# Performance work log

Measured on AMD Instinct MI355X. Metric: run time of the kernel, lower is better.

## Reference

```python
import jax, jax.numpy as jnp
import numpy as np

MEAN = 0.1307
SIGMA = 0.3081
BINARY_ITER = 10
SIG_SCALE = 5.0


def spu(x):
    # SPU(x) = x^2 - 0.5 for x >= 0, sigmoid(-x) - 1 for x < 0 (continuous at 0)
    return jnp.where(x >= 0, x * x - 0.5, jax.nn.sigmoid(-x) - 1.0)


def joining_line(x1, y1, x2, y2):
    slope = (y2 - y1) / (x2 - x1)
    return slope, y2 - slope * x2


def parabola_tangent(x):
    return 2.0 * x, -x * x - 0.5


def parabola_tangent_through(x1, y1):
    D = 4.0 * x1 * x1 - 4.0 * y1 - 2.0
    x2 = (2.0 * x1 + jnp.sqrt(jnp.clip(D, 0.0))) / 2.0
    return parabola_tangent(x2)


def sigmoid_tangent(x):
    s = jax.nn.sigmoid(x)
    slope = -s * (1.0 - s)
    return slope, -s - slope * x


def binary_search_point(lx, ux, uy):
    L = lx
    R = jnp.zeros_like(lx)
    for _ in range(BINARY_ITER):  # fixed 10-iteration search, unrolled
        m = 0.5 * (L + R)
        sm, im = sigmoid_tangent(m)
        mask = sm * ux + im - uy > 0
        L = jnp.where(mask, m, L)
        R = jnp.where(mask, R, m)
    return L


def line_to_constraint(slope, intercept):
    # [n, n+1]: diagonal slope matrix with intercept as last column (matches torch diagflat/cat)
    return jnp.concatenate([jnp.diagflat(slope), intercept[:, None]], axis=1)


def analyze_affine(W, b, ub, lb):
    constr = jnp.concatenate([W, b[:, None]], axis=1)
    bu = jnp.where(W > 0, ub[None, :], lb[None, :])
    bl = jnp.where(W > 0, lb[None, :], ub[None, :])
    return constr, jnp.einsum('ij,ij->i', bu, W) + b, jnp.einsum('ij,ij->i', bl, W) + b


def analyze_spu(ux, lx):
    uy = spu(ux)
    ly = spu(lx)
    new_ub = jnp.maximum(uy, ly)
    sj, ij = joining_line(lx, ly, ux, uy)
    right = lx > 0
    left = ux <= 0
    crossing = (~left) & (~right)
    # learned positions at their (fresh) init: sigmoid(0) -> midpoint
    mid = 0.5 * (ux + lx)
    sp, ip = parabola_tangent(mid)
    ssm, ism = sigmoid_tangent(mid)
    new_lb = jnp.where(crossing, jnp.full_like(uy, -0.5), jnp.minimum(uy, ly))
    # crossing-case lower constraint
    spu_, ipu = parabola_tangent(ux)
    limit = spu_ * lx + ipu
    clm = (jnp.abs(lx) > ux).astype(lx.dtype)
    clp = jax.nn.sigmoid((clm - 0.5) * 2.0 * SIG_SCALE) * (ly - limit) + limit
    ptm = clp < -0.5
    spt, ipt = parabola_tangent_through(lx, clp)
    sjn, ijn = joining_line(lx, clp, jnp.zeros_like(lx), jnp.full_like(lx, -0.5))
    s_cl = jnp.where(ptm, spt, sjn)
    i_cl = jnp.where(ptm, ipt, ijn)
    # crossing-case upper constraint
    ssl, isl = sigmoid_tangent(lx)
    stv = ssl * ux + isl - uy
    L = binary_search_point(lx, ux, uy)
    scp = jax.nn.sigmoid(-SIG_SCALE) * (L - lx) + lx
    ssc, isc = sigmoid_tangent(scp)
    up_mask = stv > 0
    s_cu = jnp.where(up_mask, ssc, sj)
    i_cu = jnp.where(up_mask, isc, ij)
    rf = right.astype(lx.dtype)
    lf = left.astype(lx.dtype)
    cf = crossing.astype(lx.dtype)
    us = rf * sj + lf * ssm + cf * s_cu
    ui = rf * ij + lf * ism + cf * i_cu
    ls = rf * sp + lf * sj + cf * s_cl
    li = rf * ip + lf * ij + cf * i_cl
    return line_to_constraint(us, ui), line_to_constraint(ls, li), new_ub, new_lb


def back_substitute(uc, lc, ub, lb):
    cu, cl = uc[-1], lc[-1]
    for pu, pl in zip(uc[-2::-1], lc[-2::-1]):
        # where(curr>0, prev_upper, prev_lower) contracted with curr == split pos/neg matmuls
        Wu, bu = cu[:, :-1], cu[:, -1]
        cu = jnp.maximum(Wu, 0.0) @ pu + jnp.minimum(Wu, 0.0) @ pl
        cu = cu.at[:, -1].add(bu)
        Wl, bl = cl[:, :-1], cl[:, -1]
        cl = jnp.maximum(Wl, 0.0) @ pl + jnp.minimum(Wl, 0.0) @ pu
        cl = cl.at[:, -1].add(bl)
    return jnp.minimum(ub, cu[:, 0]), jnp.maximum(lb, cl[:, 0])


def setup_inputs() -> dict:
    key = jax.random.key(0)
    ks = jax.random.split(key, 9)
    d_in, h, d_out = 784, 2048, 10
    inputs = jax.random.uniform(ks[0], (d_in,), dtype=jnp.float32)
    eps = jnp.float32(0.05)
    w1 = jax.random.normal(ks[1], (h, d_in), dtype=jnp.float32) / np.sqrt(d_in).astype(np.float32)
    b1 = jax.random.normal(ks[2], (h,), dtype=jnp.float32) * 0.1
    w2 = jax.random.normal(ks[3], (h, h), dtype=jnp.float32) / np.sqrt(h).astype(np.float32)
    b2 = jax.random.normal(ks[4], (h,), dtype=jnp.float32) * 0.1
    w3 = jax.random.normal(ks[5], (h, h), dtype=jnp.float32) / np.sqrt(h).astype(np.float32)
    b3 = jax.random.normal(ks[6], (h,), dtype=jnp.float32) * 0.1
    w4 = jax.random.normal(ks[7], (d_out, h), dtype=jnp.float32) / np.sqrt(h).astype(np.float32)
    b4 = jax.random.normal(ks[8], (d_out,), dtype=jnp.float32) * 0.1
    return {"inputs": inputs, "eps": eps, "w1": w1, "b1": b1, "w2": w2, "b2": b2,
            "w3": w3, "b3": b3, "w4": w4, "b4": b4}


def reference(inputs, eps, w1, b1, w2, b2, w3, b3, w4, b4):
    ub = [jnp.clip(inputs + eps, None, 1.0)]
    lb = [jnp.clip(inputs - eps, 0.0)]
    # normalization layer: applied in place to bounds and input constraint ([784,1])
    uc = [((ub[0] - MEAN) / SIGMA)[:, None]]
    lc = [((lb[0] - MEAN) / SIGMA)[:, None]]
    ub[0] = (ub[0] - MEAN) / SIGMA
    lb[0] = (lb[0] - MEAN) / SIGMA
    weights = [(w1, b1), (w2, b2), (w3, b3), (w4, b4)]
    for i, (W, b) in enumerate(weights):
        c, u, l = analyze_affine(W, b, ub[-1], lb[-1])
        uc.append(c)
        lc.append(c)
        ub.append(u)
        lb.append(l)
        u, l = back_substitute(uc, lc, ub[-1], lb[-1])
        ub[-1], lb[-1] = u, l
        if i < len(weights) - 1:
            cu_, cl_, u, l = analyze_spu(ub[-1], lb[-1])
            uc.append(cu_)
            lc.append(cl_)
            ub.append(u)
            lb.append(l)
            u, l = back_substitute(uc, lc, ub[-1], lb[-1])
            ub[-1], lb[-1] = u, l
    return lb[-1].min()
```

## Files before the change

kernel.cpp:

```cpp
#include <hip/hip_runtime.h>
#include <cstdint>
#include <cstddef>

#define MEAN_C 0.1307f
#define SIGMA_C 0.3081f
#define SIG_SCALE_C 5.0f

typedef __bf16 bf16_t;
typedef __bf16 bf16x8 __attribute__((ext_vector_type(8)));
typedef __bf16 bf16x4 __attribute__((ext_vector_type(4)));
typedef float f32x4 __attribute__((ext_vector_type(4)));

__device__ __forceinline__ f32x4 mfma16(bf16x8 a, bf16x8 b, f32x4 c) {
    return __builtin_amdgcn_mfma_f32_16x16x32_bf16(a, b, c, 0, 0, 0);
}

typedef const __attribute__((address_space(1))) void* gvp;
typedef __attribute__((address_space(3))) void* lvp;
__device__ __forceinline__ void g2l16(const void* g, void* l) {
    __builtin_amdgcn_global_load_lds((gvp)g, (lvp)l, 16, 0, 0);
}

__device__ __forceinline__ size_t swz(int r, int k, int ktiles) {
    return (((size_t)(r >> 4) * ktiles + (k >> 5)) << 9)
         + (((k >> 3) & 3) << 7) + ((r & 15) << 3) + (k & 7);
}

#define KTILES 64


__device__ __forceinline__ float sigmoidf_(float x) {
    if (x >= 0.f) { float e = __expf(-x); return 1.f / (1.f + e); }
    float e = __expf(x); return e / (1.f + e);
}

__device__ __forceinline__ float spu_f(float x) {
    return (x >= 0.f) ? (x * x - 0.5f) : (sigmoidf_(-x) - 1.f);
}

__device__ __forceinline__ float wave_sum(float a) {
    #pragma unroll
    for (int o = 32; o > 0; o >>= 1) a += __shfl_xor(a, o, 64);
    return a;
}

__device__ __forceinline__ void spu_body(int i, int n,
        float iUi, float iLi, float vU, float vL,
        float* __restrict__ us, float* __restrict__ ui,
        float* __restrict__ ls, float* __restrict__ li,
        float* __restrict__ pU, float* __restrict__ pL) {
    float ux = fminf(iUi, vU);
    float lx = fmaxf(iLi, vL);
    float uy = spu_f(ux), ly = spu_f(lx);
    float new_ub = fmaxf(uy, ly);
    float sj = (uy - ly) / (ux - lx);
    float ij = uy - sj * ux;
    bool right = lx > 0.f;
    bool left = ux <= 0.f;
    float mid = 0.5f * (ux + lx);
    float sp = 2.f * mid, ip = -mid * mid - 0.5f;
    float sm = sigmoidf_(mid);
    float ssm = -sm * (1.f - sm);
    float ism = -sm - ssm * mid;
    bool crossing = (!left) && (!right);
    float new_lb = crossing ? -0.5f : fminf(uy, ly);
    float spu_s = 2.f * ux, ipu = -ux * ux - 0.5f;
    float limit = spu_s * lx + ipu;
    float clm = (fabsf(lx) > ux) ? 1.f : 0.f;
    float clp = sigmoidf_((clm - 0.5f) * 2.f * SIG_SCALE_C) * (ly - limit) + limit;
    bool ptm = clp < -0.5f;
    float D = 4.f * lx * lx - 4.f * clp - 2.f;
    float x2 = (2.f * lx + sqrtf(fmaxf(D, 0.f))) * 0.5f;
    float spt = 2.f * x2, ipt = -x2 * x2 - 0.5f;
    float sjn = (clp + 0.5f) / lx;
    float ijn = -0.5f;
    float s_cl = ptm ? spt : sjn;
    float i_cl = ptm ? ipt : ijn;
    float sl = sigmoidf_(lx);
    float ssl = -sl * (1.f - sl);
    float isl = -sl - ssl * lx;
    float stv = ssl * ux + isl - uy;
    float Lb = lx, Rb = 0.f;
    #pragma unroll
    for (int t = 0; t < 10; ++t) {
        float mm = 0.5f * (Lb + Rb);
        float smm = sigmoidf_(mm);
        float sms = -smm * (1.f - smm);
        float smi = -smm - sms * mm;
        bool mask = (sms * ux + smi - uy) > 0.f;
        Lb = mask ? mm : Lb;
        Rb = mask ? Rb : mm;
    }
    float scp = sigmoidf_(-SIG_SCALE_C) * (Lb - lx) + lx;
    float sc = sigmoidf_(scp);
    float ssc = -sc * (1.f - sc);
    float isc = -sc - ssc * scp;
    bool up = stv > 0.f;
    float s_cu = up ? ssc : sj;
    float i_cu = up ? isc : ij;
    float usv, uiv, lsv, liv;
    if (right)      { usv = sj;   uiv = ij;   lsv = sp;   liv = ip;   }
    else if (left)  { usv = ssm;  uiv = ism;  lsv = sj;   liv = ij;   }
    else            { usv = s_cu; uiv = i_cu; lsv = s_cl; liv = i_cl; }
    us[i] = usv; ui[i] = uiv; ls[i] = lsv; li[i] = liv;
    float vu = (usv >= 0.f) ? vU : vL;
    float vl = (lsv >= 0.f) ? vL : vU;
    pU[i] = fminf(new_ub, usv * vu + uiv);
    pL[i] = fmaxf(new_lb, lsv * vl + liv);
}


__global__ __launch_bounds__(256) void k_interval_spu(
        const float* __restrict__ W, const float* __restrict__ b,
        const float* __restrict__ U, const float* __restrict__ L,
        int m, int n,
        float* __restrict__ us, float* __restrict__ ui,
        float* __restrict__ ls, float* __restrict__ li,
        float* __restrict__ pU, float* __restrict__ pL) {
    int r = (blockIdx.x << 2) + (threadIdx.x >> 6);
    if (r >= n) return;
    int lane = threadIdx.x & 63;
    const f32x4* Wr = (const f32x4*)(W + (size_t)r * m);
    const f32x4* U4 = (const f32x4*)U;
    const f32x4* L4 = (const f32x4*)L;
    int nf4 = m >> 2;
    float au = 0.f, al = 0.f;
    for (int j = lane; j < nf4; j += 64) {
        f32x4 wv = Wr[j], uu = U4[j], ll = L4[j];
        #pragma unroll
        for (int u = 0; u < 4; ++u) {
            float w = wv[u];
            float hi = (w > 0.f) ? uu[u] : ll[u];
            float lo2 = (w > 0.f) ? ll[u] : uu[u];
            au = fmaf(w, hi, au);
            al = fmaf(w, lo2, al);
        }
    }
    au = wave_sum(au); al = wave_sum(al);
    if (lane == 0) {
        float vU = au + b[r], vL = al + b[r];
        spu_body(r, n, vU, vL, vU, vL, us, ui, ls, li, pU, pL);
    }
}

__global__ void k_spu2(const float* __restrict__ iU, const float* __restrict__ iL,
                       const float* __restrict__ vraw, int n,
                       float* __restrict__ us, float* __restrict__ ui,
                       float* __restrict__ ls, float* __restrict__ li,
                       float* __restrict__ pU, float* __restrict__ pL) {
    int i = blockIdx.x * blockDim.x + threadIdx.x;
    if (i >= n) return;
    spu_body(i, n, iU[i], iL[i], vraw[i], vraw[n + i], us, ui, ls, li, pU, pL);
}


__global__ __launch_bounds__(256) void k_wT3(
        const float* __restrict__ W1, const float* __restrict__ W2,
        const float* __restrict__ W3,
        bf16_t* __restrict__ W1t, bf16_t* __restrict__ W2t, bf16_t* __restrict__ W3t,
        const float* __restrict__ x, const float* __restrict__ eps,
        float* __restrict__ ubn, float* __restrict__ lbn) {
    __shared__ bf16_t t[64 * 65];
    int z = blockIdx.z;
    const float* W; int N, ldw; bf16_t* Wt;
    if (z == 0)      { W = W2; N = 2048; ldw = 2048; Wt = W2t; }
    else if (z == 1) { W = W3; N = 2048; ldw = 2048; Wt = W3t; }
    else {
        W = W1; N = 784; ldw = 784; Wt = W1t;
        if (blockIdx.y >= 14) {
            if (blockIdx.y == 14 && blockIdx.x == 0) {
                for (int i = threadIdx.x; i < 896; i += 256) {
                    if (i >= 784) { ubn[i] = 0.f; lbn[i] = 0.f; }
                    else {
                        float e = eps[0];
                        float ub = fminf(x[i] + e, 1.f);
                        float lb = fmaxf(x[i] - e, 0.f);
                        ubn[i] = (ub - MEAN_C) / SIGMA_C;
                        lbn[i] = (lb - MEAN_C) / SIGMA_C;
                    }
                }
            }
            return;
        }
    }
    int k0 = blockIdx.x * 64, n0 = blockIdx.y * 64;
    int tid = threadIdx.x;
    int rg = tid >> 4;
    int cg = (tid & 15) * 4;
    bool fast = (n0 + 64 <= N);
    #pragma unroll
    for (int it = 0; it < 4; ++it) {
        int row = it * 16 + rg;
        const float* Wr = W + (size_t)(k0 + row) * ldw + n0 + cg;
        float v0, v1, v2, v3;
        if (fast) {
            f32x4 vv = *(const f32x4*)Wr;
            v0 = vv[0]; v1 = vv[1]; v2 = vv[2]; v3 = vv[3];
        } else {
            v0 = (n0 + cg + 0 < N) ? Wr[0] : 0.f;
            v1 = (n0 + cg + 1 < N) ? Wr[1] : 0.f;
            v2 = (n0 + cg + 2 < N) ? Wr[2] : 0.f;
            v3 = (n0 + cg + 3 < N) ? Wr[3] : 0.f;
        }
        t[(cg + 0) * 65 + row] = (bf16_t)v0;
        t[(cg + 1) * 65 + row] = (bf16_t)v1;
        t[(cg + 2) * 65 + row] = (bf16_t)v2;
        t[(cg + 3) * 65 + row] = (bf16_t)v3;
    }
    __syncthreads();
    #pragma unroll
    for (int p = 0; p < 2; ++p) {
        int c = tid + p * 256;
        int lr = c & 63, lq = c >> 6;
        bf16x8 v;
        #pragma unroll
        for (int u = 0; u < 8; ++u) v[u] = t[lr * 65 + lq * 8 + u];
        *(bf16x8*)(Wt + swz(n0 + lr, k0 + lq * 8, KTILES)) = v;
    }
}

__global__ __launch_bounds__(256) void k_prep16(
        const float* __restrict__ W, const float* __restrict__ b, int n,
        const float* __restrict__ cus, const float* __restrict__ cui,
        const float* __restrict__ cls, const float* __restrict__ cli,
        const float* __restrict__ bvec,
        const float* __restrict__ U, const float* __restrict__ L,
        bf16_t* __restrict__ Ab, float* __restrict__ av,
        float* __restrict__ iU, float* __restrict__ iL) {
    int rt = blockIdx.x;
    int tid = threadIdx.x, lane = tid & 63, wid = tid >> 6;
    int mrow = lane & 15, q = lane >> 4;
    int r = rt * 16 + mrow;
    bool act = r < 2 * n;
    bool isU = r < n;
    int i = act ? (isU ? r : r - n) : 0;
    float gate = act ? 1.f : 0.f;
    const float* Wr = W + (size_t)i * 2048;
    const float* ps = isU ? cus : cls;
    const float* ns = isU ? cls : cus;
    const float* yi = isU ? cui : cli;
    const float* zi = isU ? cli : cui;
    const float* hi = isU ? U : L;
    const float* lo = isU ? L : U;
    float a = 0.f, a2 = 0.f;
    bf16_t* Abase = Ab + ((size_t)rt * KTILES) * 512 + lane * 8;
    for (int kt = wid; kt < KTILES; kt += 4) {
        int k0 = kt * 32 + q * 8;
        bf16x8 ov;
        #pragma unroll
        for (int h = 0; h < 2; ++h) {
            int kb = k0 + 4 * h;
            f32x4 wv = *(const f32x4*)(Wr + kb);
            f32x4 p0 = *(const f32x4*)(ps + kb);
            f32x4 q0 = *(const f32x4*)(ns + kb);
            f32x4 y0 = *(const f32x4*)(yi + kb);
            f32x4 z0 = *(const f32x4*)(zi + kb);
            f32x4 c0 = *(const f32x4*)(bvec + kb);
            f32x4 h0 = *(const f32x4*)(hi + kb);
            f32x4 l0 = *(const f32x4*)(lo + kb);
            #pragma unroll
            for (int u = 0; u < 4; ++u) {
                float w = gate * wv[u];
                float pos = fmaxf(w, 0.f), neg = fminf(w, 0.f);
                float mx = pos * p0[u] + neg * q0[u];
                ov[4 * h + u] = (bf16_t)mx;
                a += pos * y0[u] + neg * z0[u] + mx * c0[u];
                a2 += pos * h0[u] + neg * l0[u];
            }
        }
        *(bf16x8*)(Abase + (size_t)kt * 512) = ov;
    }
    a += __shfl_xor(a, 16, 64);  a += __shfl_xor(a, 32, 64);
    a2 += __shfl_xor(a2, 16, 64); a2 += __shfl_xor(a2, 32, 64);
    __shared__ float sh[2][4][16];
    if (lane < 16) { sh[0][wid][lane] = a; sh[1][wid][lane] = a2; }
    __syncthreads();
    if (tid < 16) {
        int r2 = rt * 16 + tid;
        float ta = sh[0][0][tid] + sh[0][1][tid] + sh[0][2][tid] + sh[0][3][tid];
        float tb = sh[1][0][tid] + sh[1][1][tid] + sh[1][2][tid] + sh[1][3][tid];
        if (r2 < 2 * n) {
            bool isU2 = r2 < n;
            int i2 = isU2 ? r2 : r2 - n;
            av[r2] = ta + b[i2];
            if (isU2) iU[i2] = tb + b[i2];
            else      iL[i2] = tb + b[i2];
        } else {
            av[r2] = 0.f;
        }
    }
}

__global__ __launch_bounds__(256) void k_colmix16(
        const bf16_t* __restrict__ Cb, int ldc, int splits, size_t sstride, int n,
        int tpb,
        const float* __restrict__ cus, const float* __restrict__ cui,
        const float* __restrict__ cls, const float* __restrict__ cli,
        const float* __restrict__ bvec,
        bf16_t* __restrict__ Ab, float* __restrict__ av) {
    int rt = blockIdx.x;
    int kt0 = blockIdx.y * tpb;
    int tid = threadIdx.x, lane = tid & 63, wid = tid >> 6;
    int mrow = lane & 15, q = lane >> 4;
    int r = rt * 16 + mrow;
    bool isU = r < n;
    const bf16_t* Cr = Cb + (size_t)r * ldc;
    const float* ps = isU ? cus : cls;
    const float* ns = isU ? cls : cus;
    const float* yi = isU ? cui : cli;
    const float* zi = isU ? cli : cui;
    float a = 0.f;
    bf16_t* Abase = Ab + ((size_t)rt * KTILES) * 512 + lane * 8;
    for (int kt = kt0 + wid; kt < kt0 + tpb; kt += 4) {
        int k0 = kt * 32 + q * 8;
        float wsum[8] = {0.f, 0.f, 0.f, 0.f, 0.f, 0.f, 0.f, 0.f};
        for (int s = 0; s < splits; ++s) {
            bf16x8 v = *(const bf16x8*)(Cr + s * sstride + k0);
            #pragma unroll
            for (int u = 0; u < 8; ++u) wsum[u] += (float)v[u];
        }
        f32x4 p0 = *(const f32x4*)(ps + k0), p1 = *(const f32x4*)(ps + k0 + 4);
        f32x4 q0 = *(const f32x4*)(ns + k0), q1 = *(const f32x4*)(ns + k0 + 4);
        f32x4 y0 = *(const f32x4*)(yi + k0), y1 = *(const f32x4*)(yi + k0 + 4);
        f32x4 z0 = *(const f32x4*)(zi + k0), z1 = *(const f32x4*)(zi + k0 + 4);
        f32x4 c0 = *(const f32x4*)(bvec + k0), c1 = *(const f32x4*)(bvec + k0 + 4);
        bf16x8 ov;
        #pragma unroll
        for (int u = 0; u < 4; ++u) {
            float w = wsum[u];
            float pos = fmaxf(w, 0.f), neg = fminf(w, 0.f);
            float mx = pos * p0[u] + neg * q0[u];
            ov[u] = (bf16_t)mx;
            a += pos * y0[u] + neg * z0[u] + mx * c0[u];
        }
        #pragma unroll
        for (int u = 0; u < 4; ++u) {
            float w = wsum[4 + u];
            float pos = fmaxf(w, 0.f), neg = fminf(w, 0.f);
            float mx = pos * p1[u] + neg * q1[u];
            ov[4 + u] = (bf16_t)mx;
            a += pos * y1[u] + neg * z1[u] + mx * c1[u];
        }
        *(bf16x8*)(Abase + (size_t)kt * 512) = ov;
    }
    a += __shfl_xor(a, 16, 64);
    a += __shfl_xor(a, 32, 64);
    __shared__ float sh[4][16];
    if (lane < 16) sh[wid][lane] = a;
    __syncthreads();
    if (tid < 16) {
        float tot = sh[0][tid] + sh[1][tid] + sh[2][tid] + sh[3][tid];
        atomicAdd(&av[rt * 16 + tid], tot);
    }
}

__global__ __launch_bounds__(640) void k_reduce16f(
        const bf16_t* __restrict__ Cb, int ldc, int m, int n,
        int splits, size_t sstride,
        const float* __restrict__ av,
        const float* __restrict__ ubn, const float* __restrict__ lbn,
        const float* __restrict__ iL,
        float* __restrict__ out) {
    __shared__ float sbl[16];
    int tid = threadIdx.x, lane = tid & 63, wv = tid >> 6;
    int nch = m >> 3;
    int i = wv;
    int r = n + i;
    const bf16_t* Cr = Cb + (size_t)r * ldc;
    const float* p = lbn;
    const float* q = ubn;
    float a = 0.f;
    for (int c = lane; c < nch; c += 64) {
        float wsum[8] = {0.f, 0.f, 0.f, 0.f, 0.f, 0.f, 0.f, 0.f};
        for (int s = 0; s < splits; ++s) {
            bf16x8 v = *(const bf16x8*)(Cr + s * sstride + c * 8);
            #pragma unroll
            for (int u = 0; u < 8; ++u) wsum[u] += (float)v[u];
        }
        f32x4 p0 = *(const f32x4*)(p + c * 8), p1 = *(const f32x4*)(p + c * 8 + 4);
        f32x4 q0 = *(const f32x4*)(q + c * 8), q1 = *(const f32x4*)(q + c * 8 + 4);
        #pragma unroll
        for (int u = 0; u < 4; ++u) {
            a += fmaxf(wsum[u], 0.f) * p0[u] + fminf(wsum[u], 0.f) * q0[u];
            a += fmaxf(wsum[4 + u], 0.f) * p1[u] + fminf(wsum[4 + u], 0.f) * q1[u];
        }
    }
    a = wave_sum(a);
    if (lane == 0) sbl[i] = fmaxf(iL[i], a + av[r]);
    __syncthreads();
    if (tid < 64) {
        float v = 3.4e38f;
        for (int j = lane; j < n; j += 64) v = fminf(v, sbl[j]);
        #pragma unroll
        for (int o = 32; o > 0; o >>= 1) v = fminf(v, __shfl_down(v, o, 64));
        if (lane == 0) out[0] = v;
    }
}

#define GEMM_PIPE()                                                            \
    int tid = threadIdx.x, lane = tid & 63, w = tid >> 6;                      \
    int wm = w & 1, wn = w >> 1;                                               \
    f32x4 acc[4][4];                                                           \
    _Pragma("unroll")                                                          \
    for (int i = 0; i < 4; ++i)                                                \
        _Pragma("unroll")                                                      \
        for (int j = 0; j < 4; ++j) acc[i][j] = (f32x4){0.f, 0.f, 0.f, 0.f};   \
    auto stage = [&](int kk) {                                                 \
        int b = kk & 1;                                                        \
        size_t go = (size_t)kk * 1024;                                         \
        bf16_t* la = &As2[b * 8192 + w * 1024];                                \
        bf16_t* lb = &Bs2[b * 8192 + w * 1024];                                \
        g2l16(a0 + go, la);          g2l16(a0 + go + 512, la + 512);           \
        g2l16(a1 + go, la + 4096);   g2l16(a1 + go + 512, la + 4608);          \
        g2l16(b0 + go, lb);          g2l16(b0 + go + 512, lb + 512);           \
        g2l16(b1 + go, lb + 4096);   g2l16(b1 + go + 512, lb + 4608);          \
    };                                                                         \
    stage(0); stage(1);                                                        \
    asm volatile("s_waitcnt vmcnt(8)" ::: "memory");                           \
    __builtin_amdgcn_s_barrier();                                              \
    for (int kk = 0; kk < nk; ++kk) {                                          \
        const bf16_t* cA = &As2[(kk & 1) * 8192];                              \
        const bf16_t* cB = &Bs2[(kk & 1) * 8192];                              \
        bf16x8 af0[4], af1[4], bq0[4], bq1[4];                                 \
        _Pragma("unroll")                                                      \
        for (int i = 0; i < 4; ++i) {                                          \
            af0[i] = *(const bf16x8*)(cA + (wm * 4 + i) * 1024 + lane * 8);    \
            af1[i] = *(const bf16x8*)(cA + (wm * 4 + i) * 1024 + 512 + lane * 8); \
            bq0[i] = *(const bf16x8*)(cB + (wn * 4 + i) * 1024 + lane * 8);    \
            bq1[i] = *(const bf16x8*)(cB + (wn * 4 + i) * 1024 + 512 + lane * 8); \
        }                                                                      \
        asm volatile("s_waitcnt lgkmcnt(0)" ::: "memory");                     \
        __builtin_amdgcn_s_barrier();                                          \
        if (kk + 2 < nk) stage(kk + 2);                                        \
        _Pragma("unroll")                                                      \
        for (int i = 0; i < 4; ++i)                                            \
            _Pragma("unroll")                                                  \
            for (int j = 0; j < 4; ++j)                                        \
                acc[i][j] = mfma16(bq0[j], af0[i], acc[i][j]);                 \
        _Pragma("unroll")                                                      \
        for (int i = 0; i < 4; ++i)                                            \
            _Pragma("unroll")                                                  \
            for (int j = 0; j < 4; ++j)                                        \
                acc[i][j] = mfma16(bq1[j], af1[i], acc[i][j]);                 \
        if (kk + 2 < nk) asm volatile("s_waitcnt vmcnt(8)" ::: "memory");      \
        else             asm volatile("s_waitcnt vmcnt(0)" ::: "memory");      \
        __builtin_amdgcn_s_barrier();                                          \
    }

__global__ __launch_bounds__(256) void k_gemm16(
        const bf16_t* __restrict__ A, const bf16_t* __restrict__ Bt,
        bf16_t* __restrict__ C, int ldc, size_t sstride, int nk) {
    __shared__ __align__(16) bf16_t As2[16384];
    __shared__ __align__(16) bf16_t Bs2[16384];
    int tr0 = blockIdx.y * 8, tc0 = blockIdx.x * 8;
    int kt0 = blockIdx.z * nk * 2;
    int wtmp = threadIdx.x >> 6, ltmp = threadIdx.x & 63;
    const bf16_t* a0 = A + (((size_t)(tr0 + wtmp)     * KTILES + kt0) << 9) + ltmp * 8;
    const bf16_t* a1 = A + (((size_t)(tr0 + wtmp + 4) * KTILES + kt0) << 9) + ltmp * 8;
    const bf16_t* b0 = Bt + (((size_t)(tc0 + wtmp)     * KTILES + kt0) << 9) + ltmp * 8;
    const bf16_t* b1 = Bt + (((size_t)(tc0 + wtmp + 4) * KTILES + kt0) << 9) + ltmp * 8;
    GEMM_PIPE()
    bf16_t* Cz = C + (size_t)blockIdx.z * sstride;
    int orow = lane & 15, ocol = (lane >> 4) * 4;
    size_t row0 = (size_t)blockIdx.y * 128;
    size_t col0 = (size_t)blockIdx.x * 128;
    #pragma unroll
    for (int i = 0; i < 4; ++i) {
        size_t gr = row0 + wm * 64 + i * 16 + orow;
        #pragma unroll
        for (int j = 0; j < 4; ++j) {
            size_t gc = col0 + wn * 64 + j * 16 + ocol;
            bf16x4 v;
            #pragma unroll
            for (int rg = 0; rg < 4; ++rg) v[rg] = (bf16_t)acc[i][j][rg];
            *(bf16x4*)(Cz + gr * (size_t)ldc + gc) = v;
        }
    }
}

#define GEMM_PIPE8()                                                           \
    int tid = threadIdx.x, lane = tid & 63, w = tid >> 6;            \
    int wm = w >> 2, wn = w & 3;                                               \
    f32x4 acc[4][2];                                                           \
    _Pragma("unroll")                                                          \
    for (int i = 0; i < 4; ++i)                                                \
        _Pragma("unroll")                                                      \
        for (int j = 0; j < 2; ++j) acc[i][j] = (f32x4){0.f, 0.f, 0.f, 0.f};   \
    auto stage = [&](int kk) {                                                 \
        int b = kk & 1;                                                        \
        size_t go = (size_t)kk * 1024;                                         \
        bf16_t* la = &As2[b * 8192 + w * 1024];                                \
        bf16_t* lb = &Bs2[b * 8192 + w * 1024];                                \
        g2l16(a0 + go, la);   g2l16(a0 + go + 512, la + 512);                  \
        g2l16(b0 + go, lb);   g2l16(b0 + go + 512, lb + 512);                  \
    };                                                                         \
    stage(0); stage(1);                                                        \
    asm volatile("s_waitcnt vmcnt(4)" ::: "memory");                           \
    __builtin_amdgcn_s_barrier();                                              \
    for (int kk = 0; kk < nk; ++kk) {                                          \
        const bf16_t* cA = &As2[(kk & 1) * 8192];                              \
        const bf16_t* cB = &Bs2[(kk & 1) * 8192];                              \
        bf16x8 af0[4], af1[4], bq0[2], bq1[2];                                 \
        _Pragma("unroll")                                                      \
        for (int i = 0; i < 4; ++i) {                                          \
            af0[i] = *(const bf16x8*)(cA + (wm * 4 + i) * 1024 + lane * 8);    \
            af1[i] = *(const bf16x8*)(cA + (wm * 4 + i) * 1024 + 512 + lane * 8); \
        }                                                                      \
        _Pragma("unroll")                                                      \
        for (int j = 0; j < 2; ++j) {                                          \
            bq0[j] = *(const bf16x8*)(cB + (wn * 2 + j) * 1024 + lane * 8);    \
            bq1[j] = *(const bf16x8*)(cB + (wn * 2 + j) * 1024 + 512 + lane * 8); \
        }                                                                      \
        asm volatile("s_waitcnt lgkmcnt(0)" ::: "memory");                     \
        __builtin_amdgcn_s_barrier();                                          \
        if (kk + 2 < nk) stage(kk + 2);                                        \
        _Pragma("unroll")                                                      \
        for (int i = 0; i < 4; ++i)                                            \
            _Pragma("unroll")                                                  \
            for (int j = 0; j < 2; ++j)                                        \
                acc[i][j] = mfma16(bq0[j], af0[i], acc[i][j]);                 \
        _Pragma("unroll")                                                      \
        for (int i = 0; i < 4; ++i)                                            \
            _Pragma("unroll")                                                  \
            for (int j = 0; j < 2; ++j)                                        \
                acc[i][j] = mfma16(bq1[j], af1[i], acc[i][j]);                 \
        if (kk + 2 < nk) asm volatile("s_waitcnt vmcnt(4)" ::: "memory");      \
        else             asm volatile("s_waitcnt vmcnt(0)" ::: "memory");      \
        __builtin_amdgcn_s_barrier();                                          \
    }

__global__ __launch_bounds__(512, 4) void k_gemm16_mix(
        const bf16_t* __restrict__ A, const bf16_t* __restrict__ Bt, int n,
        const float* __restrict__ cus, const float* __restrict__ cui,
        const float* __restrict__ cls, const float* __restrict__ cli,
        const float* __restrict__ bvec,
        bf16_t* __restrict__ Ab2, float* __restrict__ av, int nk) {
    __shared__ __align__(16) bf16_t As2[16384];
    __shared__ __align__(16) bf16_t Bs2[16384];
    __shared__ float asum[4][128];
    int wg = (int)(blockIdx.y * gridDim.x + blockIdx.x);
    int xcd = wg & 7, idx = wg >> 3;
    int bm = (xcd & 3) * 8 + (idx & 7);
    int bn = (xcd >> 2) * 8 + (idx >> 3);
    int tr0 = bm * 8, tc0 = bn * 8;
    int wtmp = threadIdx.x >> 6, ltmp = threadIdx.x & 63;
    const bf16_t* a0 = A + (((size_t)(tr0 + wtmp) * KTILES) << 9) + ltmp * 8;
    const bf16_t* b0 = Bt + (((size_t)(tc0 + wtmp) * KTILES) << 9) + ltmp * 8;
    GEMM_PIPE8()
    size_t row0 = (size_t)bm * 128;
    size_t col0 = (size_t)bn * 128;
    bool isU = (int)row0 < n;
    const float* ps = isU ? cus : cls;
    const float* ns = isU ? cls : cus;
    const float* yi = isU ? cui : cli;
    const float* zi = isU ? cli : cui;
    int orow = lane & 15, ocol = (lane >> 4) * 4;
    #pragma unroll
    for (int i = 0; i < 4; ++i) {
        int gr = (int)row0 + wm * 64 + i * 16 + orow;
        float ra = 0.f;
        #pragma unroll
        for (int j = 0; j < 2; ++j) {
            int gc = (int)col0 + wn * 32 + j * 16 + ocol;
            f32x4 p0 = *(const f32x4*)(ps + gc);
            f32x4 q0 = *(const f32x4*)(ns + gc);
            f32x4 y0 = *(const f32x4*)(yi + gc);
            f32x4 z0 = *(const f32x4*)(zi + gc);
            f32x4 c0 = *(const f32x4*)(bvec + gc);
            bf16x4 ov;
            #pragma unroll
            for (int rg = 0; rg < 4; ++rg) {
                float v = acc[i][j][rg];
                float pos = fmaxf(v, 0.f), neg = fminf(v, 0.f);
                float mx = pos * p0[rg] + neg * q0[rg];
                ov[rg] = (bf16_t)mx;
                ra += pos * y0[rg] + neg * z0[rg] + mx * c0[rg];
            }
            *(bf16x4*)(Ab2 + swz(gr, gc, KTILES)) = ov;
        }
        ra += __shfl_xor(ra, 16, 64);
        ra += __shfl_xor(ra, 32, 64);
        if (lane < 16) asum[wn][wm * 64 + i * 16 + lane] = ra;
    }
    __syncthreads();
    if (tid < 128)
        atomicAdd(&av[row0 + tid],
                  asum[0][tid] + asum[1][tid] + asum[2][tid] + asum[3][tid]);
}

__global__ __launch_bounds__(256) void k_gemm16_red(
        const bf16_t* __restrict__ A, const bf16_t* __restrict__ Bt, int n,
        const float* __restrict__ ubn, const float* __restrict__ lbn,
        float* __restrict__ av, int nk) {
    __shared__ __align__(16) bf16_t As2[8192];
    __shared__ __align__(16) bf16_t Bs2[16384];
    __shared__ float asum[4][64];
    int wg = (int)blockIdx.x;
    int xcd = wg & 7, idx = wg >> 3;
    int bm = xcd * 8 + idx / 7;
    int bn = idx % 7;
    int tid = threadIdx.x, lane = tid & 63, w = tid >> 6;
    const bf16_t* aw  = A  + (((size_t)(bm * 4 + w)      * KTILES) << 9) + lane * 8;
    const bf16_t* bw0 = Bt + (((size_t)(bn * 8 + 2 * w)  * KTILES) << 9) + lane * 8;
    const bf16_t* bw1 = Bt + (((size_t)(bn * 8 + 2 * w + 1) * KTILES) << 9) + lane * 8;
    f32x4 acc[4][2];
    #pragma unroll
    for (int i = 0; i < 4; ++i)
        #pragma unroll
        for (int j = 0; j < 2; ++j) acc[i][j] = (f32x4){0.f, 0.f, 0.f, 0.f};
    auto stage = [&](int kk) {
        int b = kk & 1;
        size_t go = (size_t)kk * 1024;
        bf16_t* la = &As2[b * 4096 + w * 1024];
        bf16_t* lb = &Bs2[b * 8192 + 2 * w * 1024];
        g2l16(aw + go, la);         g2l16(aw + go + 512, la + 512);
        g2l16(bw0 + go, lb);        g2l16(bw0 + go + 512, lb + 512);
        g2l16(bw1 + go, lb + 1024); g2l16(bw1 + go + 512, lb + 1536);
    };
    stage(0); stage(1);
    asm volatile("s_waitcnt vmcnt(6)" ::: "memory");
    __builtin_amdgcn_s_barrier();
    for (int kk = 0; kk < nk; ++kk) {
        const bf16_t* cA = &As2[(kk & 1) * 4096];
        const bf16_t* cB = &Bs2[(kk & 1) * 8192];
        bf16x8 af0[4], af1[4], bq0[2], bq1[2];
        #pragma unroll
        for (int i = 0; i < 4; ++i) {
            af0[i] = *(const bf16x8*)(cA + i * 1024 + lane * 8);
            af1[i] = *(const bf16x8*)(cA + i * 1024 + 512 + lane * 8);
        }
        #pragma unroll
        for (int j = 0; j < 2; ++j) {
            bq0[j] = *(const bf16x8*)(cB + (2 * w + j) * 1024 + lane * 8);
            bq1[j] = *(const bf16x8*)(cB + (2 * w + j) * 1024 + 512 + lane * 8);
        }
        asm volatile("s_waitcnt lgkmcnt(0)" ::: "memory");
        __builtin_amdgcn_s_barrier();
        if (kk + 2 < nk) stage(kk + 2);
        #pragma unroll
        for (int i = 0; i < 4; ++i)
            #pragma unroll
            for (int j = 0; j < 2; ++j)
                acc[i][j] = mfma16(bq0[j], af0[i], acc[i][j]);
        #pragma unroll
        for (int i = 0; i < 4; ++i)
            #pragma unroll
            for (int j = 0; j < 2; ++j)
                acc[i][j] = mfma16(bq1[j], af1[i], acc[i][j]);
        if (kk + 2 < nk) asm volatile("s_waitcnt vmcnt(6)" ::: "memory");
        else             asm volatile("s_waitcnt vmcnt(0)" ::: "memory");
        __builtin_amdgcn_s_barrier();
    }
    size_t row0 = (size_t)bm * 64;
    size_t col0 = (size_t)bn * 128;
    bool isU = (int)row0 < n;
    const float* p = isU ? ubn : lbn;
    const float* q = isU ? lbn : ubn;
    int ocol = (lane >> 4) * 4;
    #pragma unroll
    for (int i = 0; i < 4; ++i) {
        float ra = 0.f;
        #pragma unroll
        for (int j = 0; j < 2; ++j) {
            int gc = (int)col0 + w * 32 + j * 16 + ocol;
            f32x4 p0 = *(const f32x4*)(p + gc);
            f32x4 q0 = *(const f32x4*)(q + gc);
            #pragma unroll
            for (int rg = 0; rg < 4; ++rg) {
                float v = acc[i][j][rg];
                ra += fmaxf(v, 0.f) * p0[rg] + fminf(v, 0.f) * q0[rg];
            }
        }
        ra += __shfl_xor(ra, 16, 64);
        ra += __shfl_xor(ra, 32, 64);
        if (lane < 16) asum[w][i * 16 + lane] = ra;
    }
    __syncthreads();
    if (tid < 64)
        atomicAdd(&av[row0 + tid],
                  asum[0][tid] + asum[1][tid] + asum[2][tid] + asum[3][tid]);
}


extern "C" void kernel_launch(void* const* d_in, const int* in_sizes, int n_in,
                              void* d_out, int out_size, void* d_ws, size_t ws_size,
                              hipStream_t stream) {
    (void)in_sizes; (void)n_in; (void)out_size; (void)ws_size;
    const float* x   = (const float*)d_in[0];
    const float* eps = (const float*)d_in[1];
    const float* W1  = (const float*)d_in[2];
    const float* B1  = (const float*)d_in[3];
    const float* W2  = (const float*)d_in[4];
    const float* B2  = (const float*)d_in[5];
    const float* W3  = (const float*)d_in[6];
    const float* B3  = (const float*)d_in[7];
    const float* W4  = (const float*)d_in[8];
    const float* B4  = (const float*)d_in[9];
    float* out = (float*)d_out;

    const int H = 2048, DIN = 784, DOUT = 10;
    const int NP1 = 896;
    const int MP4 = 128;

    float* ws = (float*)d_ws;
    size_t off = 0;
    auto alloc = [&](size_t nf) -> float* {
        float* p = ws + off;
        off += (nf + 3) & ~(size_t)3;
        return p;
    };
    float* ubn = alloc(NP1);
    float* lbn = alloc(NP1);
    float* us1 = alloc(H); float* ui1 = alloc(H); float* ls1 = alloc(H); float* li1 = alloc(H);
    float* pU1 = alloc(H); float* pL1 = alloc(H);
    float* iU2 = alloc(H); float* iL2 = alloc(H);
    float* us2 = alloc(H); float* ui2 = alloc(H); float* ls2 = alloc(H); float* li2 = alloc(H);
    float* pU2 = alloc(H); float* pL2 = alloc(H);
    float* iU3 = alloc(H); float* iL3 = alloc(H);
    float* us3 = alloc(H); float* ui3 = alloc(H); float* ls3 = alloc(H); float* li3 = alloc(H);
    float* pU3 = alloc(H); float* pL3 = alloc(H);
    float* iU4 = alloc(32); float* iL4 = alloc(32);
    float* av  = alloc(2 * H);
    bf16_t* Ab  = (bf16_t*)alloc((size_t)2 * H * H / 2);
    bf16_t* Ab2 = (bf16_t*)alloc((size_t)2 * H * H / 2);
    bf16_t* W1t = (bf16_t*)alloc((size_t)NP1 * H / 2);
    bf16_t* W2t = (bf16_t*)alloc((size_t)H * H / 2);
    bf16_t* W3t = (bf16_t*)alloc((size_t)H * H / 2);
    bf16_t* Cs  = (bf16_t*)alloc((size_t)16 * MP4 * H / 2);

    dim3 blk(256);

    k_wT3<<<dim3(32, 32, 3), blk, 0, stream>>>(W1, W2, W3, W1t, W2t, W3t,
                                               x, eps, ubn, lbn);

    size_t ss4H = (size_t)MP4 * H;
    size_t ss4N = (size_t)MP4 * NP1;

    k_interval_spu<<<dim3(H / 4), blk, 0, stream>>>(W1, B1, ubn, lbn, DIN, H,
        us1, ui1, ls1, li1, pU1, pL1);

    k_prep16<<<dim3(2 * H / 16), blk, 0, stream>>>(W2, B2, H,
        us1, ui1, ls1, li1, B1, pU1, pL1, Ab, av, iU2, iL2);
    k_gemm16_red<<<dim3(448), blk, 0, stream>>>(Ab, W1t, H,
        ubn, lbn, av, KTILES / 2);
    k_spu2<<<dim3(H / 64), dim3(64), 0, stream>>>(iU2, iL2, av, H,
        us2, ui2, ls2, li2, pU2, pL2);

    k_prep16<<<dim3(2 * H / 16), blk, 0, stream>>>(W3, B3, H,
        us2, ui2, ls2, li2, B2, pU2, pL2, Ab, av, iU3, iL3);
    k_gemm16_mix<<<dim3(2 * H / 128, H / 128), dim3(512), 0, stream>>>(Ab, W2t, H,
        us1, ui1, ls1, li1, B1, Ab2, av, KTILES / 2);
    k_gemm16_red<<<dim3(448), blk, 0, stream>>>(Ab2, W1t, H,
        ubn, lbn, av, KTILES / 2);
    k_spu2<<<dim3(H / 64), dim3(64), 0, stream>>>(iU3, iL3, av, H,
        us3, ui3, ls3, li3, pU3, pL3);

    k_prep16<<<dim3(MP4 / 16), blk, 0, stream>>>(W4, B4, DOUT,
        us3, ui3, ls3, li3, B3, pU3, pL3, Ab, av, iU4, iL4);
    k_gemm16<<<dim3(H / 128, MP4 / 128, 16), blk, 0, stream>>>(Ab, W3t, Cs, H, ss4H, 2);
    k_colmix16<<<dim3(MP4 / 16, 8), blk, 0, stream>>>(Cs, H, 16, ss4H, DOUT, KTILES / 8,
        us2, ui2, ls2, li2, B2, Ab2, av);
    k_gemm16<<<dim3(H / 128, MP4 / 128, 16), blk, 0, stream>>>(Ab2, W2t, Cs, H, ss4H, 2);
    k_colmix16<<<dim3(MP4 / 16, 8), blk, 0, stream>>>(Cs, H, 16, ss4H, DOUT, KTILES / 8,
        us1, ui1, ls1, li1, B1, Ab, av);
    k_gemm16<<<dim3(NP1 / 128, MP4 / 128, 16), blk, 0, stream>>>(Ab, W1t, Cs, NP1, ss4N, 2);
    k_reduce16f<<<dim3(1), dim3(640), 0, stream>>>(Cs, NP1, DIN, DOUT, 16, ss4N,
        av, ubn, lbn, iL4, out);
}
```

Measured before the change: 321.9 us.

## Use narrow 32-row GEMM tile for final-layer back-substitution chain

Replaces the 128x128-tile GEMM used in the last-layer back-substitution with a specialized kernel whose M tile is 32 rows, since only 2*DOUT=20 constraint rows are needed. The padded row count MP4 drops from 128 to 32, so the A operand, the prep/colmix launches and the MFMA work shrink roughly fourfold. Each wave now computes a 32x32 output block and streams more of B per block. The risk is lower arithmetic intensity on the B loads and smaller per-wave work.

Result: faster. 311.5 us (-3.2%).

```diff
diff --git a/kernel.cpp b/kernel.cpp
--- a/kernel.cpp
+++ b/kernel.cpp
@@ -397,83 +397,74 @@
     }
 }
 
-#define GEMM_PIPE()                                                            \
-    int tid = threadIdx.x, lane = tid & 63, w = tid >> 6;                      \
-    int wm = w & 1, wn = w >> 1;                                               \
-    f32x4 acc[4][4];                                                           \
-    _Pragma("unroll")                                                          \
-    for (int i = 0; i < 4; ++i)                                                \
-        _Pragma("unroll")                                                      \
-        for (int j = 0; j < 4; ++j) acc[i][j] = (f32x4){0.f, 0.f, 0.f, 0.f};   \
-    auto stage = [&](int kk) {                                                 \
-        int b = kk & 1;                                                        \
-        size_t go = (size_t)kk * 1024;                                         \
-        bf16_t* la = &As2[b * 8192 + w * 1024];                                \
-        bf16_t* lb = &Bs2[b * 8192 + w * 1024];                                \
-        g2l16(a0 + go, la);          g2l16(a0 + go + 512, la + 512);           \
-        g2l16(a1 + go, la + 4096);   g2l16(a1 + go + 512, la + 4608);          \
-        g2l16(b0 + go, lb);          g2l16(b0 + go + 512, lb + 512);           \
-        g2l16(b1 + go, lb + 4096);   g2l16(b1 + go + 512, lb + 4608);          \
-    };                                                                         \
-    stage(0); stage(1);                                                        \
-    asm volatile("s_waitcnt vmcnt(8)" ::: "memory");                           \
-    __builtin_amdgcn_s_barrier();                                              \
-    for (int kk = 0; kk < nk; ++kk) {                                          \
-        const bf16_t* cA = &As2[(kk & 1) * 8192];                              \
-        const bf16_t* cB = &Bs2[(kk & 1) * 8192];                              \
-        bf16x8 af0[4], af1[4], bq0[4], bq1[4];                                 \
-        _Pragma("unroll")                                                      \
-        for (int i = 0; i < 4; ++i) {                                          \
-            af0[i] = *(const bf16x8*)(cA + (wm * 4 + i) * 1024 + lane * 8);    \
-            af1[i] = *(const bf16x8*)(cA + (wm * 4 + i) * 1024 + 512 + lane * 8); \
-            bq0[i] = *(const bf16x8*)(cB + (wn * 4 + i) * 1024 + lane * 8);    \
-            bq1[i] = *(const bf16x8*)(cB + (wn * 4 + i) * 1024 + 512 + lane * 8); \
-        }                                                                      \
-        asm volatile("s_waitcnt lgkmcnt(0)" ::: "memory");                     \
-        __builtin_amdgcn_s_barrier();                                          \
-        if (kk + 2 < nk) stage(kk + 2);                                        \
-        _Pragma("unroll")                                                      \
-        for (int i = 0; i < 4; ++i)                                            \
-            _Pragma("unroll")                                                  \
-            for (int j = 0; j < 4; ++j)                                        \
-                acc[i][j] = mfma16(bq0[j], af0[i], acc[i][j]);                 \
-        _Pragma("unroll")                                                      \
-        for (int i = 0; i < 4; ++i)                                            \
-            _Pragma("unroll")                                                  \
-            for (int j = 0; j < 4; ++j)                                        \
-                acc[i][j] = mfma16(bq1[j], af1[i], acc[i][j]);                 \
-        if (kk + 2 < nk) asm volatile("s_waitcnt vmcnt(8)" ::: "memory");      \
-        else             asm volatile("s_waitcnt vmcnt(0)" ::: "memory");      \
-        __builtin_amdgcn_s_barrier();                                          \
-    }
-
-__global__ __launch_bounds__(256) void k_gemm16(
+__global__ __launch_bounds__(256) void k_gemm16s(
         const bf16_t* __restrict__ A, const bf16_t* __restrict__ Bt,
         bf16_t* __restrict__ C, int ldc, size_t sstride, int nk) {
-    __shared__ __align__(16) bf16_t As2[16384];
-    __shared__ __align__(16) bf16_t Bs2[16384];
-    int tr0 = blockIdx.y * 8, tc0 = blockIdx.x * 8;
+    __shared__ __align__(16) bf16_t As2[8192];
+    __shared__ __align__(16) bf16_t Bs2[32768];
+    int bn = blockIdx.x;
     int kt0 = blockIdx.z * nk * 2;
-    int wtmp = threadIdx.x >> 6, ltmp = threadIdx.x & 63;
-    const bf16_t* a0 = A + (((size_t)(tr0 + wtmp)     * KTILES + kt0) << 9) + ltmp * 8;
-    const bf16_t* a1 = A + (((size_t)(tr0 + wtmp + 4) * KTILES + kt0) << 9) + ltmp * 8;
-    const bf16_t* b0 = Bt + (((size_t)(tc0 + wtmp)     * KTILES + kt0) << 9) + ltmp * 8;
-    const bf16_t* b1 = Bt + (((size_t)(tc0 + wtmp + 4) * KTILES + kt0) << 9) + ltmp * 8;
-    GEMM_PIPE()
+    int tid = threadIdx.x, lane = tid & 63, w = tid >> 6;
+    const bf16_t* aw = A +
+        (((size_t)(w >> 1) * KTILES + kt0 + (w & 1)) << 9) + lane * 8;
+    const bf16_t* bt0 = Bt +
+        (((size_t)(bn * 8 + 2 * w) * KTILES + kt0) << 9) + lane * 8;
+    const bf16_t* bt1 = Bt +
+        (((size_t)(bn * 8 + 2 * w + 1) * KTILES + kt0) << 9) + lane * 8;
+    f32x4 acc[2][2];
+    #pragma unroll
+    for (int i = 0; i < 2; ++i)
+        #pragma unroll
+        for (int j = 0; j < 2; ++j) acc[i][j] = (f32x4){0.f, 0.f, 0.f, 0.f};
+    auto stage = [&](int kk) {
+        int b = kk & 1;
+        size_t go = (size_t)kk * 1024;
+        g2l16(aw + go,        &As2[b * 4096 + w * 1024]);
+        g2l16(bt0 + go,       &Bs2[b * 16384 + (4 * w + 0) * 1024]);
+        g2l16(bt0 + go + 512, &Bs2[b * 16384 + (4 * w + 1) * 1024]);
+        g2l16(bt1 + go,       &Bs2[b * 16384 + (4 * w + 2) * 1024]);
+        g2l16(bt1 + go + 512, &Bs2[b * 16384 + (4 * w + 3) * 1024]);
+    };
+    stage(0); stage(1);
+    asm volatile("s_waitcnt vmcnt(5)" ::: "memory");
+    __builtin_amdgcn_s_barrier();
+    for (int kk = 0; kk < nk; ++kk) {
+        const bf16_t* cA = &As2[(kk & 1) * 4096];
+        const bf16_t* cB = &Bs2[(kk & 1) * 16384];
+        bf16x8 af[2][2], bq[2][2];
+        #pragma unroll
+        for (int i = 0; i < 2; ++i)
+            #pragma unroll
+            for (int h = 0; h < 2; ++h) {
+                af[i][h] = *(const bf16x8*)(cA + (i * 2 + h) * 1024 + lane * 8);
+                bq[i][h] = *(const bf16x8*)(cB + (4 * w + i * 2 + h) * 1024 + lane * 8);
+            }
+        asm volatile("s_waitcnt lgkmcnt(0)" ::: "memory");
+        __builtin_amdgcn_s_barrier();
+        if (kk + 2 < nk) stage(kk + 2);
+        #pragma unroll
+        for (int h = 0; h < 2; ++h)
+            #pragma unroll
+            for (int i = 0; i < 2; ++i)
+                #pragma unroll
+                for (int j = 0; j < 2; ++j)
+                    acc[i][j] = mfma16(bq[j][h], af[i][h], acc[i][j]);
+        if (kk + 2 < nk) asm volatile("s_waitcnt vmcnt(5)" ::: "memory");
+        else             asm volatile("s_waitcnt vmcnt(0)" ::: "memory");
+        __builtin_amdgcn_s_barrier();
+    }
     bf16_t* Cz = C + (size_t)blockIdx.z * sstride;
     int orow = lane & 15, ocol = (lane >> 4) * 4;
-    size_t row0 = (size_t)blockIdx.y * 128;
-    size_t col0 = (size_t)blockIdx.x * 128;
-    #pragma unroll
-    for (int i = 0; i < 4; ++i) {
-        size_t gr = row0 + wm * 64 + i * 16 + orow;
-        #pragma unroll
-        for (int j = 0; j < 4; ++j) {
-            size_t gc = col0 + wn * 64 + j * 16 + ocol;
+    #pragma unroll
+    for (int i = 0; i < 2; ++i) {
+        int gr = i * 16 + orow;
+        #pragma unroll
+        for (int j = 0; j < 2; ++j) {
+            int gc = bn * 128 + w * 32 + j * 16 + ocol;
             bf16x4 v;
             #pragma unroll
             for (int rg = 0; rg < 4; ++rg) v[rg] = (bf16_t)acc[i][j][rg];
-            *(bf16x4*)(Cz + gr * (size_t)ldc + gc) = v;
+            *(bf16x4*)(Cz + (size_t)gr * ldc + gc) = v;
         }
     }
 }
@@ -700,7 +691,7 @@
 
     const int H = 2048, DIN = 784, DOUT = 10;
     const int NP1 = 896;
-    const int MP4 = 128;
+    const int MP4 = 32;
 
     float* ws = (float*)d_ws;
     size_t off = 0;
@@ -757,13 +748,13 @@
 
     k_prep16<<<dim3(MP4 / 16), blk, 0, stream>>>(W4, B4, DOUT,
         us3, ui3, ls3, li3, B3, pU3, pL3, Ab, av, iU4, iL4);
-    k_gemm16<<<dim3(H / 128, MP4 / 128, 16), blk, 0, stream>>>(Ab, W3t, Cs, H, ss4H, 2);
+    k_gemm16s<<<dim3(H / 128, 1, 16), blk, 0, stream>>>(Ab, W3t, Cs, H, ss4H, 2);
     k_colmix16<<<dim3(MP4 / 16, 8), blk, 0, stream>>>(Cs, H, 16, ss4H, DOUT, KTILES / 8,
         us2, ui2, ls2, li2, B2, Ab2, av);
-    k_gemm16<<<dim3(H / 128, MP4 / 128, 16), blk, 0, stream>>>(Ab2, W2t, Cs, H, ss4H, 2);
+    k_gemm16s<<<dim3(H / 128, 1, 16), blk, 0, stream>>>(Ab2, W2t, Cs, H, ss4H, 2);
     k_colmix16<<<dim3(MP4 / 16, 8), blk, 0, stream>>>(Cs, H, 16, ss4H, DOUT, KTILES / 8,
         us1, ui1, ls1, li1, B1, Ab, av);
-    k_gemm16<<<dim3(NP1 / 128, MP4 / 128, 16), blk, 0, stream>>>(Ab, W1t, Cs, NP1, ss4N, 2);
+    k_gemm16s<<<dim3(NP1 / 128, 1, 16), blk, 0, stream>>>(Ab, W1t, Cs, NP1, ss4N, 2);
     k_reduce16f<<<dim3(1), dim3(640), 0, stream>>>(Cs, NP1, DIN, DOUT, 16, ss4N,
         av, ubn, lbn, iL4, out);
 }
```
